# Kernel tuning notes

Hardware: AMD Instinct MI355X
Metric: run time of the kernel (lower is better)

Reference implementation:

```python
import jax, jax.numpy as jnp
import numpy as np

B, L, H = 16, 96, 150
WED, PED = 100, 50
EMB = WED + PED  # 150
WV, TV = 50000, 50


def setup_inputs() -> dict:
    key = jax.random.key(0)
    ks = jax.random.split(key, 16)
    f = lambda k, shape, s=0.1: jax.random.normal(k, shape, dtype=jnp.float32) * s
    return {
        "words_idx_tensor": jax.random.randint(ks[0], (B, L), 0, WV),
        "pos_idx_tensor": jax.random.randint(ks[1], (B, L), 0, TV),
        "max_length": L,
        "word_emb": f(ks[2], (WV, WED)),
        "tag_emb": f(ks[3], (TV, PED)),
        "W_ih0": f(ks[4], (2, 4 * H, EMB)),        # layer 0, both dirs
        "W_ih_rest": f(ks[5], (3, 2, 4 * H, 2 * H)),  # layers 1-3
        "W_hh": f(ks[6], (4, 2, 4 * H, H)),
        "b_ih": f(ks[7], (4, 2, 4 * H)),
        "b_hh": f(ks[8], (4, 2, 4 * H)),
        "w1": jax.random.uniform(ks[9], (1,), jnp.float32, -1.0, 1.0),
        "w2": jax.random.uniform(ks[10], (1,), jnp.float32, -1.0, 1.0),
        "w3": jax.random.uniform(ks[11], (1,), jnp.float32, -1.0, 1.0),
        "w4": jax.random.uniform(ks[12], (1,), jnp.float32, -1.0, 1.0),
        "mlp_w1": f(ks[13], (100, 4 * H)),
        "mlp_b1": jnp.zeros((100,), jnp.float32),
        "mlp_w2": f(ks[14], (1, 100)),
        "mlp_b2": jnp.zeros((1,), jnp.float32),
    }


def _lstm_dir(x, Wih, Whh, bi, bh):
    # x: [B, T, D] -> hidden states [B, T, H]; torch LSTM cell math (gate order i,f,g,o)
    Bx = x.shape[0]
    Hh = Whh.shape[-1]
    pre = jnp.einsum('btd,gd->btg', x, Wih) + bi + bh  # input contribution, [B,T,4H]

    def step(carry, p):
        h, c = carry
        gates = p + h @ Whh.T
        i, fg, g, o = jnp.split(gates, 4, axis=-1)
        i, fg, o = jax.nn.sigmoid(i), jax.nn.sigmoid(fg), jax.nn.sigmoid(o)
        g = jnp.tanh(g)
        c = fg * c + i * g
        h = o * jnp.tanh(c)
        return (h, c), h

    init = (jnp.zeros((Bx, Hh), x.dtype), jnp.zeros((Bx, Hh), x.dtype))
    _, hs = jax.lax.scan(step, init, pre.transpose(1, 0, 2))  # [T,B,H]
    return hs.transpose(1, 0, 2)


def _bilstm(x, W_ih0, W_ih_rest, W_hh, b_ih, b_hh):
    inp = x
    for layer in range(4):  # fixed structural loop over layers
        outs = []
        for d in range(2):  # forward / backward direction
            Wih = W_ih0[d] if layer == 0 else W_ih_rest[layer - 1, d]
            xs = inp if d == 0 else inp[:, ::-1]
            hs = _lstm_dir(xs, Wih, W_hh[layer, d], b_ih[layer, d], b_hh[layer, d])
            outs.append(hs if d == 0 else hs[:, ::-1])
        inp = jnp.concatenate(outs, axis=-1)  # [B,T,2H]
    return inp


def reference(words_idx_tensor, pos_idx_tensor, max_length, word_emb, tag_emb,
              W_ih0, W_ih_rest, W_hh, b_ih, b_hh, w1, w2, w3, w4,
              mlp_w1, mlp_b1, mlp_w2, mlp_b2):
    we = word_emb[words_idx_tensor[:, :max_length]]   # [B,L,WED]
    te = tag_emb[pos_idx_tensor[:, :max_length]]      # [B,L,PED]
    embeds = jnp.concatenate([we, te], axis=-1)       # [B,L,EMB]
    out = _bilstm(embeds, W_ih0, W_ih_rest, W_hh, b_ih, b_hh)  # [B,L,2H]
    Bn, Lm, C = out.shape
    # features[l1, b, l2] = cat(out[b, l1], out[b, l2])  -> [L, B, L, 4H]
    ht = out.transpose(1, 0, 2)  # [L,B,2H]
    head = jnp.broadcast_to(ht[:, :, None, :], (Lm, Bn, Lm, C))
    dep = jnp.broadcast_to(out[None, :, :, :], (Lm, Bn, Lm, C))
    features = jnp.concatenate([head, dep], axis=-1)  # [L,B,L,4H]
    # w1*f + w2*f^2 + w3*f^3 + w4*f^4 via Horner (single fused elementwise pass)
    poly = features * (w1[0] + features * (w2[0] + features * (w3[0] + features * w4[0])))
    h1 = jnp.tanh(poly @ mlp_w1.T + mlp_b1)           # [L,B,L,100]
    edge_scores = h1 @ mlp_w2.T + mlp_b2              # [L,B,L,1]
    return edge_scores
```

## Files before the change

### kernel.cpp

```cpp
#include <hip/hip_runtime.h>

typedef __attribute__((ext_vector_type(8))) _Float16 half8;
typedef __attribute__((ext_vector_type(4))) _Float16 half4;
typedef __attribute__((ext_vector_type(4))) float float4v;
typedef __attribute__((ext_vector_type(2))) float float2v;

__device__ __forceinline__ float4v mfma16h(half8 a, half8 b, float4v c) {
  return __builtin_amdgcn_mfma_f32_16x16x32_f16(a, b, c, 0, 0, 0);
}

__device__ __forceinline__ half8 cat44h(half4 a, half4 b) {
  half8 r;
  r[0]=a[0]; r[1]=a[1]; r[2]=a[2]; r[3]=a[3];
  r[4]=b[0]; r[5]=b[1]; r[6]=b[2]; r[7]=b[3];
  return r;
}

__device__ __forceinline__ void split_f16(float x, _Float16& hi, _Float16& lo) {
  hi = (_Float16)x;
  lo = (_Float16)(x - (float)hi);
}

#define KLOG2E 1.442695041f
__device__ __forceinline__ float fast_tanh(float x) {
  float z = __builtin_amdgcn_exp2f(2.f * KLOG2E * x);
  return 1.f - 2.f * __builtin_amdgcn_rcpf(1.f + z);
}


__global__ void prep_kernel(
    const float* __restrict__ Wih0,
    const float* __restrict__ WihR,
    const float* __restrict__ Whh,
    const float* __restrict__ bih,
    const float* __restrict__ bhh,
    const float* __restrict__ w1m,
    const float* __restrict__ b1v,
    const int* __restrict__ widx, const int* __restrict__ pidx,
    const float* __restrict__ wemb, const float* __restrict__ temb,
    _Float16* __restrict__ whh_f,
    _Float16* __restrict__ wih_f,
    _Float16* __restrict__ wpr_f,
    float* __restrict__ bsum, float* __restrict__ b1cat,
    _Float16* __restrict__ xa)
{
  const int N_whh  = 8 * 40 * 5 * 512;
  const int N_wih0 = 2 * 40 * 5 * 512;
  const int N_wihr = 6 * 40 * 10 * 512;
  const int N_wpr  = 16 * 10 * 512;
  const int N_bs   = 8 * 640;
  const int N_emb  = 1536 * 320;
  const int total  = N_whh + N_wih0 + N_wihr + N_wpr + N_bs + 256 + N_emb;
  for (int i = blockIdx.x * blockDim.x + threadIdx.x; i < total;
       i += gridDim.x * blockDim.x) {
    int idx = i;
    if (idx < N_whh) {
      int e = idx & 7, lane = (idx >> 3) & 63, r = idx >> 9;
      int kc = r % 5; r /= 5; int nt = r % 40; int ld = r / 40;
      int jrow = (nt >> 2) * 16 + (lane & 15);
      int g = (nt & 3) * 150 + jrow;
      int k = 32 * kc + 16 * (e >> 2) + 4 * (lane >> 4) + (e & 3);
      float v = (jrow < 150 && k < 150) ? Whh[((size_t)ld * 600 + g) * 150 + k] : 0.f;
      v *= ((nt & 3) == 2) ? (2.f * KLOG2E) : (-KLOG2E);
      whh_f[idx] = (_Float16)v;
      continue;
    }
    idx -= N_whh;
    if (idx < N_wih0) {
      int e = idx & 7, lane = (idx >> 3) & 63, r = idx >> 9;
      int kc = r % 5; r /= 5; int nt = r % 40; int dir = r / 40;
      int jrow = (nt >> 2) * 16 + (lane & 15);
      int g = (nt & 3) * 150 + jrow;
      int k = 32 * kc + 16 * (e >> 2) + 4 * (lane >> 4) + (e & 3);
      float v = (jrow < 150 && k < 150) ? Wih0[((size_t)dir * 600 + g) * 150 + k] : 0.f;
      v *= ((nt & 3) == 2) ? (2.f * KLOG2E) : (-KLOG2E);
      wih_f[idx] = (_Float16)v;
      continue;
    }
    idx -= N_wih0;
    if (idx < N_wihr) {
      int e = idx & 7, lane = (idx >> 3) & 63, r = idx >> 9;
      int kc = r % 10; r /= 10; int nt = r % 40; int ld = r / 40;
      int jrow = (nt >> 2) * 16 + (lane & 15);
      int g = (nt & 3) * 150 + jrow;
      int k = 32 * kc + 16 * (e >> 2) + 4 * (lane >> 4) + (e & 3);
      int ks = (k < 150) ? k : ((k >= 160 && k < 310) ? (k - 10) : -1);
      float v = (jrow < 150 && ks >= 0) ? WihR[((size_t)ld * 600 + g) * 300 + ks] : 0.f;
      v *= ((nt & 3) == 2) ? (2.f * KLOG2E) : (-KLOG2E);
      wih_f[N_wih0 + idx] = (_Float16)v;
      continue;
    }
    idx -= N_wihr;
    if (idx < N_wpr) {
      int e = idx & 7, lane = (idx >> 3) & 63, r = idx >> 9;
      int kc = r % 10; int nt = r / 10;
      int ko = 16 * nt + (lane & 15);
      int k = 32 * kc + 16 * (e >> 2) + 4 * (lane >> 4) + (e & 3);
      int ks = (k < 150) ? k : ((k >= 160 && k < 310) ? (k - 10) : -1);
      float v = 0.f;
      if (ks >= 0) {
        if (ko < 100) v = w1m[(size_t)ko * 600 + ks];
        else if (ko < 200) v = w1m[(size_t)(ko - 100) * 600 + 300 + ks];
      }
      wpr_f[idx] = (_Float16)v;
      continue;
    }
    idx -= N_wpr;
    if (idx < N_bs) {
      int ld = idx / 640, gp = idx - 640 * ld;
      int nt = gp >> 4, lrow = gp & 15;
      int jrow = (nt >> 2) * 16 + lrow;
      int g = (nt & 3) * 150 + jrow;
      float v = (jrow < 150) ? bih[ld * 600 + g] + bhh[ld * 600 + g] : 0.f;
      v *= ((nt & 3) == 2) ? (2.f * KLOG2E) : (-KLOG2E);
      bsum[idx] = v;
      continue;
    }
    idx -= N_bs;
    if (idx < 256) {
      b1cat[idx] = (idx < 100) ? b1v[idx] : ((idx < 200) ? b1v[idx - 100] : 0.f);
      continue;
    }
    idx -= 256;
    {
      int row = idx / 320, j = idx - 320 * row;
      int b = row & 15, t = row >> 4;
      float v = 0.f;
      if (j < 100) v = wemb[(size_t)widx[b * 96 + t] * 100 + j];
      else if (j < 150) v = temb[(size_t)pidx[b * 96 + t] * 50 + (j - 100)];
      xa[idx] = (_Float16)v;
    }
  }
}

template <int KC>
__global__ __launch_bounds__(512) void pregemm_kernel(
    const _Float16* __restrict__ x_h,
    const _Float16* __restrict__ wih_f,
    const float* __restrict__ bsum_l,
    float* __restrict__ pre)
{
  const int t = blockIdx.x, dir = blockIdx.y;
  const int tid = threadIdx.x, wv = tid >> 6, lane = tid & 63;
  const int lrow = lane & 15, lgrp = lane >> 4;
  const _Float16* wf = wih_f + (size_t)dir * 40 * KC * 512;
  float4v acc[5];
#pragma unroll
  for (int tt = 0; tt < 5; ++tt) acc[tt] = (float4v){0.f, 0.f, 0.f, 0.f};
  const size_t arow = ((size_t)t * 16 + lrow) * 320;
#pragma unroll
  for (int kc = 0; kc < KC; ++kc) {
    int co = 32 * kc + 4 * lgrp;
    half8 ah = cat44h(*(const half4*)(x_h + arow + co),
                      *(const half4*)(x_h + arow + co + 16));
#pragma unroll
    for (int tt = 0; tt < 5; ++tt) {
      int nt = 5 * wv + tt;
      const size_t wo = ((size_t)(nt * KC + kc) * 64 + lane) * 8;
      half8 bw = *(const half8*)(wf + wo);
      acc[tt] = mfma16h(ah, bw, acc[tt]);
    }
  }
  float* po = pre + (size_t)(dir * 96 + t) * 10240;
  const float* bs = bsum_l + dir * 640;
#pragma unroll
  for (int tt = 0; tt < 5; ++tt) {
    int nt = 5 * wv + tt;
    float bv = bs[16 * nt + lrow];
    float4v v;
#pragma unroll
    for (int jj = 0; jj < 4; ++jj) v[jj] = acc[tt][jj] + bv;
    int tid_s = (nt >> 2) * 64 + lgrp * 16 + lrow;
    *(float4v*)(po + (size_t)tid_s * 16 + (nt & 3) * 4) = v;
  }
}

__global__ __launch_bounds__(640, 1) void scan_kernel(
    const float* __restrict__ pre,
    const _Float16* __restrict__ whh_f,
    _Float16* __restrict__ xo,
    int layer)
{
  const int dir = blockIdx.x;
  const int tid = threadIdx.x, wv = tid >> 6, lane = tid & 63;
  const int lrow = lane & 15, lgrp = lane >> 4;

  __shared__ __align__(16) _Float16 hb[2][16 * 172];

  for (int i = tid; i < 2 * 16 * 172; i += 640)
    (&hb[0][0])[i] = (_Float16)0.f;

  const _Float16* b_base = whh_f + (size_t)(layer * 2 + dir) * 40 * 5 * 512;
  half8 Bw[4][5];
#pragma unroll
  for (int tt = 0; tt < 4; ++tt)
#pragma unroll
    for (int kc = 0; kc < 5; ++kc) {
      size_t o = ((size_t)((4 * wv + tt) * 5 + kc) * 64 + lane) * 8;
      Bw[tt][kc] = *(const half8*)(b_base + o);
    }

  float2v cst01 = {0.f, 0.f}, cst23 = {0.f, 0.f};
  const int j = 16 * wv + lrow;
  const int kcj = j >> 5, wj = j & 31;
  const int hoff = kcj * 32 + ((wj >> 2) & 3) * 8 + (wj >> 4) * 4 + (wj & 3);

  const int t0 = dir ? 95 : 0;
  const long pincv = dir ? -2560 : 2560;
  const long xinc = dir ? -(16 * 320) : (16 * 320);
  const float4v* pc = (const float4v*)pre + ((size_t)(dir * 96 + t0) * 640 + tid) * 4;
  _Float16* xop = xo + ((size_t)t0 * 16 + 4 * lgrp) * 320 + dir * 160 + j;

  float4v pfA[4], pfB[4];
#pragma unroll
  for (int i = 0; i < 4; ++i) pfA[i] = pc[i];
  pc += pincv;
#pragma unroll
  for (int i = 0; i < 4; ++i) pfB[i] = pc[i];
  pc += pincv;

  _Float16 hsA0 = 0, hsA1 = 0, hsA2 = 0, hsA3 = 0;
  _Float16 hsB0 = 0, hsB1 = 0, hsB2 = 0, hsB3 = 0;
  __syncthreads();

#define GATE_PAIR(PF, J0, J1, CST, HVO)                                   \
  {                                                                       \
    float2v zi = {__builtin_amdgcn_exp2f(PF[0][J0]),                      \
                  __builtin_amdgcn_exp2f(PF[0][J1])};                     \
    float2v zf = {__builtin_amdgcn_exp2f(PF[1][J0]),                      \
                  __builtin_amdgcn_exp2f(PF[1][J1])};                     \
    float2v zg = {__builtin_amdgcn_exp2f(PF[2][J0]),                      \
                  __builtin_amdgcn_exp2f(PF[2][J1])};                     \
    float2v zo = {__builtin_amdgcn_exp2f(PF[3][J0]),                      \
                  __builtin_amdgcn_exp2f(PF[3][J1])};                     \
    float2v tq = (1.f + zi) * (zg + 1.f);                                 \
    float2v fq = 1.f + zf;                                                \
    float2v Dq = tq * fq;                                                 \
    float2v Nq = CST * tq + (zg - 1.f) * fq;                              \
    float rP = __builtin_amdgcn_rcpf(Dq[0] * Dq[1]);                      \
    float2v Dsw = __builtin_shufflevector(Dq, Dq, 1, 0);                  \
    float2v cv = Nq * rP * Dsw;                                           \
    CST = cv;                                                             \
    float2v arg = (2.f * KLOG2E) * cv;                                    \
    float2v zc = {__builtin_amdgcn_exp2f(arg[0]),                         \
                  __builtin_amdgcn_exp2f(arg[1])};                        \
    float2v Eq = (1.f + zo) * (zc + 1.f);                                 \
    float rE = __builtin_amdgcn_rcpf(Eq[0] * Eq[1]);                      \
    float2v Esw = __builtin_shufflevector(Eq, Eq, 1, 0);                  \
    HVO = (zc - 1.f) * rE * Esw;                                          \
  }

#define SCAN_STEP(PF, H0, H1, H2, H3, O0, O1, O2, O3, HIN, HOUT)          \
  {                                                                       \
    asm volatile("" :: "v"(O0), "v"(O1), "v"(O2), "v"(O3));               \
    __builtin_amdgcn_s_setprio(1);                                        \
    _Pragma("unroll")                                                     \
    for (int kc = 0; kc < 5; ++kc) {                                      \
      const int ao = lrow * 172 + kc * 32 + lgrp * 8;                     \
      half8 ah = *(const half8*)((HIN) + ao);                             \
      _Pragma("unroll")                                                   \
      for (int tt = 0; tt < 4; ++tt)                                      \
        PF[tt] = mfma16h(ah, Bw[tt][kc], PF[tt]);                         \
    }                                                                     \
    __builtin_amdgcn_s_setprio(0);                                        \
    float2v hv01, hv23;                                                   \
    GATE_PAIR(PF, 0, 1, cst01, hv01)                                      \
    GATE_PAIR(PF, 2, 3, cst23, hv23)                                      \
    H0 = (_Float16)hv01[0];                                               \
    H1 = (_Float16)hv01[1];                                               \
    H2 = (_Float16)hv23[0];                                               \
    H3 = (_Float16)hv23[1];                                               \
    (HOUT)[(4 * lgrp + 0) * 172 + hoff] = H0;                             \
    (HOUT)[(4 * lgrp + 1) * 172 + hoff] = H1;                             \
    (HOUT)[(4 * lgrp + 2) * 172 + hoff] = H2;                             \
    (HOUT)[(4 * lgrp + 3) * 172 + hoff] = H3;                             \
    xop[0 * 320] = H0; xop[1 * 320] = H1;                                 \
    xop[2 * 320] = H2; xop[3 * 320] = H3;                                 \
    _Pragma("unroll")                                                     \
    for (int i = 0; i < 4; ++i) PF[i] = pc[i];                            \
    pc += pincv;                                                          \
    xop += xinc;                                                          \
    asm volatile("s_waitcnt lgkmcnt(0)" ::: "memory");                    \
    __builtin_amdgcn_s_barrier();                                         \
  }

#pragma unroll 1
  for (int s2 = 0; s2 < 48; ++s2) {
    SCAN_STEP(pfA, hsA0, hsA1, hsA2, hsA3, hsB0, hsB1, hsB2, hsB3, hb[0], hb[1]);
    SCAN_STEP(pfB, hsB0, hsB1, hsB2, hsB3, hsA0, hsA1, hsA2, hsA3, hb[1], hb[0]);
  }
#undef SCAN_STEP
#undef GATE_PAIR
}

__global__ __launch_bounds__(512) void proj_kernel(
    const _Float16* __restrict__ xi,
    const _Float16* __restrict__ wpr_f,
    const float* __restrict__ b1cat,
    const float* __restrict__ w1, const float* __restrict__ w2,
    const float* __restrict__ w3, const float* __restrict__ w4,
    float* __restrict__ AD)
{
  const int t = blockIdx.x;
  const int tid = threadIdx.x, wv = tid >> 6, lane = tid & 63;
  const int lrow = lane & 15, lgrp = lane >> 4;
  __shared__ __align__(16) _Float16 ph[16 * 328];
  __shared__ __align__(16) _Float16 pl[16 * 328];
  {
    float c1 = w1[0], c2 = w2[0], c3 = w3[0], c4 = w4[0];
    for (int e = tid; e < 16 * 320; e += 512) {
      int row = e / 320, col = e - 320 * row;
      float x = (float)xi[(size_t)t * 5120 + e];
      float p = x * (c1 + x * (c2 + x * (c3 + x * c4)));
      _Float16 h, l; split_f16(p, h, l);
      ph[row * 328 + col] = h; pl[row * 328 + col] = l;
    }
  }
  __syncthreads();
  float4v acc[2] = {{0.f, 0.f, 0.f, 0.f}, {0.f, 0.f, 0.f, 0.f}};
#pragma unroll
  for (int kc = 0; kc < 10; ++kc) {
    int co = lrow * 328 + 32 * kc + 4 * lgrp;
    half8 ah = cat44h(*(const half4*)(ph + co), *(const half4*)(ph + co + 16));
    half8 al = cat44h(*(const half4*)(pl + co), *(const half4*)(pl + co + 16));
#pragma unroll
    for (int tt = 0; tt < 2; ++tt) {
      int nt = 2 * wv + tt;
      size_t wo = ((size_t)(nt * 10 + kc) * 64 + lane) * 8;
      half8 bw = *(const half8*)(wpr_f + wo);
      acc[tt] = mfma16h(ah, bw, acc[tt]);
      acc[tt] = mfma16h(al, bw, acc[tt]);
    }
  }
#pragma unroll
  for (int tt = 0; tt < 2; ++tt) {
    int ko = 16 * (2 * wv + tt) + lrow;
    float bv = b1cat[ko];
#pragma unroll
    for (int jj = 0; jj < 4; ++jj)
      AD[((size_t)t * 16 + 4 * lgrp + jj) * 256 + ko] = acc[tt][jj] + bv;
  }
}

__global__ __launch_bounds__(768) void combine_kernel(
    const float* __restrict__ AD, const float* __restrict__ w2v,
    const float* __restrict__ b2v, float* __restrict__ out)
{
  const int bb = blockIdx.x & 15, lt = blockIdx.x >> 4;
  const int tid = threadIdx.x;
  __shared__ float Dl[100 * 97];
  __shared__ float Al[100 * 9];
  __shared__ float w2s[100];
  for (int i = tid; i < 96 * 32; i += 768) {
    int ld = i >> 5, f4 = i & 31;
    if (f4 < 25) {
      float4v v = *(const float4v*)(AD + ((size_t)ld * 16 + bb) * 256 + 100 + 4 * f4);
      int k0 = 4 * f4;
      Dl[(k0 + 0) * 97 + ld] = v[0];
      Dl[(k0 + 1) * 97 + ld] = v[1];
      Dl[(k0 + 2) * 97 + ld] = v[2];
      Dl[(k0 + 3) * 97 + ld] = v[3];
    }
  }
  for (int i = tid; i < 8 * 32; i += 768) {
    int lh = i >> 5, f4 = i & 31;
    if (f4 < 25) {
      int lseq = lt * 8 + lh;
      float4v v = *(const float4v*)(AD + ((size_t)lseq * 16 + bb) * 256 + 4 * f4);
      int k0 = 4 * f4;
      Al[(k0 + 0) * 9 + lh] = v[0];
      Al[(k0 + 1) * 9 + lh] = v[1];
      Al[(k0 + 2) * 9 + lh] = v[2];
      Al[(k0 + 3) * 9 + lh] = v[3];
    }
  }
  if (tid < 100) w2s[tid] = w2v[tid];
  __syncthreads();
  int lh = tid / 96, ld = tid - 96 * lh;
  float s = 0.f;
#pragma unroll 4
  for (int k = 0; k < 100; ++k) {
    float x = Al[k * 9 + lh] + Dl[k * 97 + ld];
    s += w2s[k] * fast_tanh(x);
  }
  out[((size_t)(lt * 8 + lh) * 16 + bb) * 96 + ld] = s + b2v[0];
}

extern "C" void kernel_launch(void* const* d_in, const int* in_sizes, int n_in,
                              void* d_out, int out_size, void* d_ws, size_t ws_size,
                              hipStream_t stream)
{
  const int*   widx = (const int*)d_in[0];
  const int*   pidx = (const int*)d_in[1];
  const float* wemb = (const float*)d_in[3];
  const float* temb = (const float*)d_in[4];
  const float* Wih0 = (const float*)d_in[5];
  const float* WihR = (const float*)d_in[6];
  const float* Whh  = (const float*)d_in[7];
  const float* bih  = (const float*)d_in[8];
  const float* bhh  = (const float*)d_in[9];
  const float* w1   = (const float*)d_in[10];
  const float* w2   = (const float*)d_in[11];
  const float* w3   = (const float*)d_in[12];
  const float* w4   = (const float*)d_in[13];
  const float* w1m  = (const float*)d_in[14];
  const float* b1v  = (const float*)d_in[15];
  const float* w2m  = (const float*)d_in[16];
  const float* b2v  = (const float*)d_in[17];
  float* out = (float*)d_out;

  char* ws = (char*)d_ws;
  size_t off = 0;
  auto alloc = [&](size_t bytes) -> char* {
    char* p = ws + off;
    off = (off + bytes + 255) & ~(size_t)255;
    return p;
  };
  _Float16* WHH_F = (_Float16*)alloc(819200ull * 2);
  _Float16* WIH_F = (_Float16*)alloc(1433600ull * 2);
  _Float16* WPR_F = (_Float16*)alloc(81920ull * 2);
  float* BSUM = (float*)alloc(5120ull * 4);
  float* B1C  = (float*)alloc(256ull * 4);
  _Float16* XA = (_Float16*)alloc(491520ull * 2);
  _Float16* XB = (_Float16*)alloc(491520ull * 2);
  float* PRE = (float*)alloc(1966080ull * 4);
  float* AD  = (float*)alloc(1536ull * 256 * 4);

  prep_kernel<<<512, 256, 0, stream>>>(Wih0, WihR, Whh, bih, bhh, w1m, b1v,
      widx, pidx, wemb, temb,
      WHH_F, WIH_F, WPR_F, BSUM, B1C, XA);

  for (int layer = 0; layer < 4; ++layer) {
    const _Float16* xin = (layer & 1) ? XB : XA;
    _Float16* xout = (layer & 1) ? XA : XB;
    const float* bsl = BSUM + layer * 2 * 640;
    if (layer == 0) {
      pregemm_kernel<5><<<dim3(96, 2), 512, 0, stream>>>(xin, WIH_F, bsl, PRE);
    } else {
      size_t wo = 204800ull + (size_t)(layer - 1) * 409600ull;
      pregemm_kernel<10><<<dim3(96, 2), 512, 0, stream>>>(xin, WIH_F + wo, bsl, PRE);
    }
    scan_kernel<<<2, 640, 0, stream>>>(PRE, WHH_F, xout, layer);
  }
  proj_kernel<<<96, 512, 0, stream>>>(XA, WPR_F, B1C, w1, w2, w3, w4, AD);
  combine_kernel<<<192, 768, 0, stream>>>(AD, w2m, b2v, out);
}
```

Baseline: 490.1 us.

## Shrink LSTM scan block to eight waves, redistributing leftover gate tiles via LDS

The recurrent scan kernel now runs 512 threads (8 waves) per direction instead of 640. Each wave takes one extra MFMA output tile, and those tile results are staged through shared memory so all 512 threads compute the leftover 32 hidden units' gates. The pre-gemm output layout is changed to a 20-float stride per thread to feed the fifth accumulator. The aim is fewer waves per barrier and cheaper synchronization on the serial recurrence. The cost is an extra LDS round trip and a second barrier in every time step.

After: 575.0 us. 1.17x slower.

```diff
diff --git a/kernel.cpp b/kernel.cpp
--- a/kernel.cpp
+++ b/kernel.cpp
@@ -170,12 +170,14 @@
     float4v v;
 #pragma unroll
     for (int jj = 0; jj < 4; ++jj) v[jj] = acc[tt][jj] + bv;
-    int tid_s = (nt >> 2) * 64 + lgrp * 16 + lrow;
-    *(float4v*)(po + (size_t)tid_s * 16 + (nt & 3) * 4) = v;
-  }
-}
-
-__global__ __launch_bounds__(640, 1) void scan_kernel(
+    int sc_tid, slot;
+    if (nt < 32) { sc_tid = (nt >> 2) * 64 + lgrp * 16 + lrow; slot = (nt & 3) * 4; }
+    else         { sc_tid = (nt - 32) * 64 + lgrp * 16 + lrow; slot = 16; }
+    *(float4v*)(po + (size_t)sc_tid * 20 + slot) = v;
+  }
+}
+
+__global__ __launch_bounds__(512, 1) void scan_kernel(
     const float* __restrict__ pre,
     const _Float16* __restrict__ whh_f,
     _Float16* __restrict__ xo,
@@ -186,12 +188,13 @@
   const int lrow = lane & 15, lgrp = lane >> 4;
 
   __shared__ __align__(16) _Float16 hb[2][16 * 172];
-
-  for (int i = tid; i < 2 * 16 * 172; i += 640)
+  __shared__ float gXl[16 * 132];
+
+  for (int i = tid; i < 2 * 16 * 172; i += 512)
     (&hb[0][0])[i] = (_Float16)0.f;
 
   const _Float16* b_base = whh_f + (size_t)(layer * 2 + dir) * 40 * 5 * 512;
-  half8 Bw[4][5];
+  half8 Bw[4][5], BwX[5];
 #pragma unroll
   for (int tt = 0; tt < 4; ++tt)
 #pragma unroll
@@ -199,28 +202,38 @@
       size_t o = ((size_t)((4 * wv + tt) * 5 + kc) * 64 + lane) * 8;
       Bw[tt][kc] = *(const half8*)(b_base + o);
     }
+#pragma unroll
+  for (int kc = 0; kc < 5; ++kc) {
+    size_t o = ((size_t)((32 + wv) * 5 + kc) * 64 + lane) * 8;
+    BwX[kc] = *(const half8*)(b_base + o);
+  }
 
   float2v cst01 = {0.f, 0.f}, cst23 = {0.f, 0.f};
+  float cstX = 0.f;
   const int j = 16 * wv + lrow;
   const int kcj = j >> 5, wj = j & 31;
   const int hoff = kcj * 32 + ((wj >> 2) & 3) * 8 + (wj >> 4) * 4 + (wj & 3);
+  const int bX = tid >> 5, jjX = tid & 31;
+  const int hoffX = 128 + ((jjX >> 2) & 3) * 8 + (jjX >> 4) * 4 + (jjX & 3);
+  const int gxw = (wv & 3) * 32 + 16 * (wv >> 2) + lrow;
 
   const int t0 = dir ? 95 : 0;
-  const long pincv = dir ? -2560 : 2560;
+  const long pincv = dir ? -10240 : 10240;
   const long xinc = dir ? -(16 * 320) : (16 * 320);
-  const float4v* pc = (const float4v*)pre + ((size_t)(dir * 96 + t0) * 640 + tid) * 4;
-  _Float16* xop = xo + ((size_t)t0 * 16 + 4 * lgrp) * 320 + dir * 160 + j;
-
-  float4v pfA[4], pfB[4];
-#pragma unroll
-  for (int i = 0; i < 4; ++i) pfA[i] = pc[i];
+  const float* pc = pre + (size_t)(dir * 96 + t0) * 10240 + (size_t)tid * 20;
+  _Float16* xop  = xo + ((size_t)t0 * 16 + 4 * lgrp) * 320 + dir * 160 + j;
+  _Float16* xopX = xo + ((size_t)t0 * 16 + bX) * 320 + dir * 160 + 128 + jjX;
+
+  float4v pfA[5], pfB[5];
+#pragma unroll
+  for (int i = 0; i < 5; ++i) pfA[i] = *(const float4v*)(pc + 4 * i);
   pc += pincv;
 #pragma unroll
-  for (int i = 0; i < 4; ++i) pfB[i] = pc[i];
+  for (int i = 0; i < 5; ++i) pfB[i] = *(const float4v*)(pc + 4 * i);
   pc += pincv;
 
-  _Float16 hsA0 = 0, hsA1 = 0, hsA2 = 0, hsA3 = 0;
-  _Float16 hsB0 = 0, hsB1 = 0, hsB2 = 0, hsB3 = 0;
+  _Float16 hsA0 = 0, hsA1 = 0, hsA2 = 0, hsA3 = 0, hsA4 = 0;
+  _Float16 hsB0 = 0, hsB1 = 0, hsB2 = 0, hsB3 = 0, hsB4 = 0;
   __syncthreads();
 
 #define GATE_PAIR(PF, J0, J1, CST, HVO)                                   \
@@ -250,22 +263,48 @@
     HVO = (zc - 1.f) * rE * Esw;                                          \
   }
 
-#define SCAN_STEP(PF, H0, H1, H2, H3, O0, O1, O2, O3, HIN, HOUT)          \
+#define SCAN_STEP(PF, H0, H1, H2, H3, H4, O0, O1, O2, O3, O4, HIN, HOUT)  \
   {                                                                       \
-    asm volatile("" :: "v"(O0), "v"(O1), "v"(O2), "v"(O3));               \
+    asm volatile("" :: "v"(O0), "v"(O1), "v"(O2), "v"(O3), "v"(O4));      \
     __builtin_amdgcn_s_setprio(1);                                        \
     _Pragma("unroll")                                                     \
     for (int kc = 0; kc < 5; ++kc) {                                      \
       const int ao = lrow * 172 + kc * 32 + lgrp * 8;                     \
       half8 ah = *(const half8*)((HIN) + ao);                             \
+      PF[4] = mfma16h(ah, BwX[kc], PF[4]);                                \
       _Pragma("unroll")                                                   \
       for (int tt = 0; tt < 4; ++tt)                                      \
         PF[tt] = mfma16h(ah, Bw[tt][kc], PF[tt]);                         \
     }                                                                     \
     __builtin_amdgcn_s_setprio(0);                                        \
+    _Pragma("unroll")                                                     \
+    for (int jj = 0; jj < 4; ++jj)                                        \
+      gXl[(4 * lgrp + jj) * 132 + gxw] = PF[4][jj];                       \
+    asm volatile("s_waitcnt lgkmcnt(0)" ::: "memory");                    \
+    __builtin_amdgcn_s_barrier();                                         \
+    asm volatile("" ::: "memory");                                        \
     float2v hv01, hv23;                                                   \
     GATE_PAIR(PF, 0, 1, cst01, hv01)                                      \
     GATE_PAIR(PF, 2, 3, cst23, hv23)                                      \
+    {                                                                     \
+      float g0 = gXl[bX * 132 + 0 * 32 + jjX];                            \
+      float g1 = gXl[bX * 132 + 1 * 32 + jjX];                            \
+      float g2 = gXl[bX * 132 + 2 * 32 + jjX];                            \
+      float g3 = gXl[bX * 132 + 3 * 32 + jjX];                            \
+      float zi = __builtin_amdgcn_exp2f(g0);                              \
+      float zf = __builtin_amdgcn_exp2f(g1);                              \
+      float zg = __builtin_amdgcn_exp2f(g2);                              \
+      float zo = __builtin_amdgcn_exp2f(g3);                              \
+      float tq = (1.f + zi) * (zg + 1.f);                                 \
+      float fq = 1.f + zf;                                                \
+      float cX = (cstX * tq + (zg - 1.f) * fq) *                          \
+                 __builtin_amdgcn_rcpf(tq * fq);                          \
+      cstX = cX;                                                          \
+      float zc = __builtin_amdgcn_exp2f(2.f * KLOG2E * cX);               \
+      float hX = (zc - 1.f) *                                             \
+                 __builtin_amdgcn_rcpf((1.f + zo) * (zc + 1.f));          \
+      H4 = (_Float16)hX;                                                  \
+    }                                                                     \
     H0 = (_Float16)hv01[0];                                               \
     H1 = (_Float16)hv01[1];                                               \
     H2 = (_Float16)hv23[0];                                               \
@@ -274,20 +313,26 @@
     (HOUT)[(4 * lgrp + 1) * 172 + hoff] = H1;                             \
     (HOUT)[(4 * lgrp + 2) * 172 + hoff] = H2;                             \
     (HOUT)[(4 * lgrp + 3) * 172 + hoff] = H3;                             \
+    (HOUT)[bX * 172 + hoffX] = H4;                                        \
     xop[0 * 320] = H0; xop[1 * 320] = H1;                                 \
     xop[2 * 320] = H2; xop[3 * 320] = H3;                                 \
+    xopX[0] = H4;                                                         \
     _Pragma("unroll")                                                     \
-    for (int i = 0; i < 4; ++i) PF[i] = pc[i];                            \
+    for (int i = 0; i < 5; ++i) PF[i] = *(const float4v*)(pc + 4 * i);    \
     pc += pincv;                                                          \
     xop += xinc;                                                          \
+    xopX += xinc;                                                         \
     asm volatile("s_waitcnt lgkmcnt(0)" ::: "memory");                    \
     __builtin_amdgcn_s_barrier();                                         \
+    asm volatile("" ::: "memory");                                        \
   }
 
 #pragma unroll 1
   for (int s2 = 0; s2 < 48; ++s2) {
-    SCAN_STEP(pfA, hsA0, hsA1, hsA2, hsA3, hsB0, hsB1, hsB2, hsB3, hb[0], hb[1]);
-    SCAN_STEP(pfB, hsB0, hsB1, hsB2, hsB3, hsA0, hsA1, hsA2, hsA3, hb[1], hb[0]);
+    SCAN_STEP(pfA, hsA0, hsA1, hsA2, hsA3, hsA4,
+              hsB0, hsB1, hsB2, hsB3, hsB4, hb[0], hb[1]);
+    SCAN_STEP(pfB, hsB0, hsB1, hsB2, hsB3, hsB4,
+              hsA0, hsA1, hsA2, hsA3, hsA4, hb[1], hb[0]);
   }
 #undef SCAN_STEP
 #undef GATE_PAIR
@@ -440,7 +485,7 @@
       size_t wo = 204800ull + (size_t)(layer - 1) * 409600ull;
       pregemm_kernel<10><<<dim3(96, 2), 512, 0, stream>>>(xin, WIH_F + wo, bsl, PRE);
     }
-    scan_kernel<<<2, 640, 0, stream>>>(PRE, WHH_F, xout, layer);
+    scan_kernel<<<2, 512, 0, stream>>>(PRE, WHH_F, xout, layer);
   }
   proj_kernel<<<96, 512, 0, stream>>>(XA, WPR_F, B1C, w1, w2, w3, w4, AD);
   combine_kernel<<<192, 768, 0, stream>>>(AD, w2m, b2v, out);
```
